# Optimization experiments

Hardware: AMD Instinct MI355X
Metric: run time of the kernel (lower is better)

## Reference

```python
import jax, jax.numpy as jnp
import numpy as np

N, DIM, K = 65536, 512, 256


def setup_inputs() -> dict:
    key = jax.random.key(0)
    k1, k2 = jax.random.split(key)
    embeddings = jax.random.normal(k1, (N, DIM), dtype=jnp.float32)
    # Centroid table produced by the (external, non-differentiable) faiss
    # k-means fit; materialized here as a learned parameter.
    centroids = jax.random.normal(k2, (K, DIM), dtype=jnp.float32)
    return {"embeddings": embeddings, "centroids": centroids, "batch_id": 0}


def reference(embeddings, centroids, batch_id):
    # Batched equivalent of the Python loop over samples:
    # for each embedding, cdist to centroids, take the 2nd-nearest centroid.
    # Squared L2 preserves the ordering of torch.cdist (monotone sqrt),
    # and the output is a gather of centroids, so math is identical.
    # d2: [N, K]
    d2 = (
        jnp.sum(embeddings * embeddings, axis=1, keepdims=True)
        - 2.0 * jnp.einsum("nd,kd->nk", embeddings, centroids)
        + jnp.sum(centroids * centroids, axis=1)
    )
    # top-2 smallest distances -> indices of nearest and 2nd-nearest centroids
    _, top2_idx = jax.lax.top_k(-d2, 2)  # [N, 2]
    hard_neg_idx = top2_idx[:, 1]  # second-nearest centroid per sample
    return centroids[hard_neg_idx]  # [N, DIM]
```

## Files before the change

### kernel.cpp

```cpp
#include <hip/hip_runtime.h>

#define N_EMB 65536
#define DIM   512
#define K_C   256
#define ROWS  128
#define NCHUNK (DIM / 32)


typedef __attribute__((ext_vector_type(4))) float        f32x4;
typedef __attribute__((ext_vector_type(8))) __bf16       bf16x8;
typedef __attribute__((ext_vector_type(8))) short        s16x8;
typedef __attribute__((ext_vector_type(4))) unsigned int u32x4;

template <class T>
__device__ inline auto mfma_bf16_t(T a, T b, f32x4 c, int)
    -> decltype(__builtin_amdgcn_mfma_f32_16x16x32_bf16(a, b, c, 0, 0, 0)) {
  return __builtin_amdgcn_mfma_f32_16x16x32_bf16(a, b, c, 0, 0, 0);
}
template <class T>
__device__ inline f32x4 mfma_bf16_t(T a, T b, f32x4 c, long) {
  return __builtin_amdgcn_mfma_f32_16x16x32_bf16(
      __builtin_bit_cast(s16x8, a), __builtin_bit_cast(s16x8, b), c, 0, 0, 0);
}
__device__ inline f32x4 MFMA(bf16x8 a, bf16x8 b, f32x4 c) {
  return mfma_bf16_t(a, b, c, 0);
}

__device__ inline unsigned umin_(unsigned a, unsigned b) { return a < b ? a : b; }
__device__ inline unsigned umax_(unsigned a, unsigned b) { return a > b ? a : b; }

__device__ inline void cvt8(const float4 a, const float4 b, u32x4& hw, u32x4& lw) {
  float v[8] = {a.x, a.y, a.z, a.w, b.x, b.y, b.z, b.w};
  unsigned h[8], l[8];
#pragma unroll
  for (int i = 0; i < 8; ++i) {
    const unsigned u  = __float_as_uint(v[i]);
    const unsigned hb = (u + 0x7FFFu + ((u >> 16) & 1u)) >> 16;
    h[i] = hb;
    const float hf = __uint_as_float(hb << 16);
    const unsigned ul = __float_as_uint(v[i] - hf);
    l[i] = (ul + 0x7FFFu + ((ul >> 16) & 1u)) >> 16;
  }
  hw = (u32x4){h[0] | (h[1] << 16), h[2] | (h[3] << 16),
               h[4] | (h[5] << 16), h[6] | (h[7] << 16)};
  lw = (u32x4){l[0] | (l[1] << 16), l[2] | (l[3] << 16),
               l[4] | (l[5] << 16), l[6] | (l[7] << 16)};
}

__device__ inline u32x4 cvt8hi(const float4 a, const float4 b) {
  float v[8] = {a.x, a.y, a.z, a.w, b.x, b.y, b.z, b.w};
  unsigned h[8];
#pragma unroll
  for (int i = 0; i < 8; ++i) {
    const unsigned u = __float_as_uint(v[i]);
    h[i] = (u + 0x7FFFu + ((u >> 16) & 1u)) >> 16;
  }
  return (u32x4){h[0] | (h[1] << 16), h[2] | (h[3] << 16),
                 h[4] | (h[5] << 16), h[6] | (h[7] << 16)};
}

__global__ void pack_centroids(const float* __restrict__ cent,
                               unsigned* __restrict__ cbh,
                               float* __restrict__ cnorm) {
  const int k    = blockIdx.x;
  const int lane = threadIdx.x;
  const float* src = cent + (size_t)k * DIM + lane * 8;
  const float4 a = *(const float4*)src;
  const float4 b = *(const float4*)(src + 4);
  const int chunk = lane >> 2, g = lane & 3;
  ((u32x4*)cbh)[((size_t)chunk * 16 + (k >> 4)) * 64 + g * 16 + (k & 15)] =
      cvt8hi(a, b);
  float s = a.x * a.x + a.y * a.y + a.z * a.z + a.w * a.w +
            b.x * b.x + b.y * b.y + b.z * b.z + b.w * b.w;
#pragma unroll
  for (int off = 32; off > 0; off >>= 1) s += __shfl_down(s, off, 64);
  if (lane == 0) cnorm[k] = s;
}

__global__ __launch_bounds__(256, 2)
void neg_sampler_main(const float* __restrict__ emb,
                      const float* __restrict__ cent,
                      const unsigned* __restrict__ cbh,
                      const float* __restrict__ cnorm,
                      float* __restrict__ out) {
  extern __shared__ char lds[];
  char* const EH = lds;
  char* const EL = lds + 8192;
  char* const CB = lds + 16384;

  const int tid  = threadIdx.x;
  const int lane = tid & 63;
  const int w    = tid >> 6;
  const int row0 = blockIdx.x * ROWS;

  f32x4 acc[2][16];
#pragma unroll
  for (int i = 0; i < 2; ++i)
#pragma unroll
    for (int j = 0; j < 16; ++j) acc[i][j] = (f32x4){0.f, 0.f, 0.f, 0.f};

  const int er = tid & 127;
  const int g0 = (tid >> 7) * 2;
  const float* const ebase = emb + (size_t)(row0 + er) * DIM;
  const int et = er >> 4, erow = er & 15;
  const int eoffA = et * 1024 + (g0 * 16 + erow) * 16;
  const int eoffB = et * 1024 + ((g0 + 1) * 16 + erow) * 16;

  float4 ev0, ev1, ev2, ev3;
  u32x4  cv0, cv1, cv2, cv3;

  auto load_chunk = [&](int c) {
    const float* p0 = ebase + c * 32 + g0 * 8;
    ev0 = *(const float4*)p0;
    ev1 = *(const float4*)(p0 + 4);
    ev2 = *(const float4*)(p0 + 8);
    ev3 = *(const float4*)(p0 + 12);
    const u32x4* cs = (const u32x4*)cbh + (size_t)c * 1024 + tid;
    cv0 = cs[0]; cv1 = cs[256]; cv2 = cs[512]; cv3 = cs[768];
  };
  auto store_chunk = [&]() {
    u32x4 hw, lw;
    cvt8(ev0, ev1, hw, lw);
    *(u32x4*)(EH + eoffA) = hw; *(u32x4*)(EL + eoffA) = lw;
    cvt8(ev2, ev3, hw, lw);
    *(u32x4*)(EH + eoffB) = hw; *(u32x4*)(EL + eoffB) = lw;
    u32x4* cd = (u32x4*)CB + tid;
    cd[0] = cv0; cd[256] = cv1; cd[512] = cv2; cd[768] = cv3;
  };

  load_chunk(0);
  for (int c = 0; c < NCHUNK; ++c) {
    if (c) __syncthreads();
    store_chunk();
    if (c < NCHUNK - 1) load_chunk(c + 1);
    asm volatile("s_waitcnt lgkmcnt(0)" ::: "memory");
    __builtin_amdgcn_sched_barrier(0);
    __builtin_amdgcn_s_barrier();
    asm volatile("" ::: "memory");

    const char* ehp = EH + (2 * w) * 1024 + lane * 16;
    const char* elp = EL + (2 * w) * 1024 + lane * 16;
    const bf16x8 eh0 = *(const bf16x8*)ehp;
    const bf16x8 eh1 = *(const bf16x8*)(ehp + 1024);
    const bf16x8 el0 = *(const bf16x8*)elp;
    const bf16x8 el1 = *(const bf16x8*)(elp + 1024);
    const char* cbp = CB + lane * 16;
#pragma unroll
    for (int ct = 0; ct < 16; ++ct) {
      const bf16x8 ch = *(const bf16x8*)(cbp + ct * 1024);
      acc[0][ct] = MFMA(eh0, ch, acc[0][ct]);
      acc[1][ct] = MFMA(eh1, ch, acc[1][ct]);
      acc[0][ct] = MFMA(el0, ch, acc[0][ct]);
      acc[1][ct] = MFMA(el1, ch, acc[1][ct]);
    }
  }
  __syncthreads();

  unsigned* top4 = (unsigned*)lds;
  const int lgrp = lane >> 4, lcol = lane & 15;
  float cnv[16];
#pragma unroll
  for (int ct = 0; ct < 16; ++ct) cnv[ct] = cnorm[ct * 16 + lcol];

#pragma unroll
  for (int rt = 0; rt < 2; ++rt) {
#pragma unroll
    for (int rg = 0; rg < 4; ++rg) {
      unsigned b0 = 0xFFFFFFFFu, b1 = b0, b2 = b0, b3 = b0;
      auto ins = [&](unsigned u) {
        b3 = umin_(b3, umax_(b2, u));
        b2 = umin_(b2, umax_(b1, u));
        b1 = umin_(b1, umax_(b0, u));
        b0 = umin_(b0, u);
      };
#pragma unroll
      for (int ct = 0; ct < 16; ++ct) {
        const float s = fmaf(-2.f, acc[rt][ct][rg], cnv[ct]);
        ins((__float_as_uint(s) & 0xFFFFFF00u) | (unsigned)(ct * 16 + lcol));
      }
#pragma unroll
      for (int off = 1; off < 16; off <<= 1) {
        const unsigned o0 = __shfl_xor(b0, off, 64);
        const unsigned o1 = __shfl_xor(b1, off, 64);
        const unsigned o2 = __shfl_xor(b2, off, 64);
        const unsigned o3 = __shfl_xor(b3, off, 64);
        ins(o0); ins(o1); ins(o2); ins(o3);
      }
      if (lcol == 0) {
        const int row = w * 32 + rt * 16 + lgrp * 4 + rg;
        *(u32x4*)(top4 + row * 4) = (u32x4){b0, b1, b2, b3};
      }
    }
  }
  __syncthreads();

  for (int rr = 0; rr < 32; ++rr) {
    const int row  = w * 32 + rr;
    const int grow = row0 + row;
    const unsigned t0 = top4[row * 4 + 0], t1 = top4[row * 4 + 1];
    const unsigned t2 = top4[row * 4 + 2], t3 = top4[row * 4 + 3];
    const int c0 = (int)(t0 & 0xFFu), c1 = (int)(t1 & 0xFFu);
    const int c2 = (int)(t2 & 0xFFu), c3 = (int)(t3 & 0xFFu);
    const int cj = lane >> 4, li = lane & 15;
    const int myc = cj == 0 ? c0 : cj == 1 ? c1 : cj == 2 ? c2 : c3;

    const float4* e4 = (const float4*)(emb + (size_t)grow * DIM);
    const float4* c4 = (const float4*)(cent + (size_t)myc * DIM);
    float d = 0.f;
#pragma unroll
    for (int i = 0; i < 8; ++i) {
      const float4 ev = e4[li + 16 * i];
      const float4 cv = c4[li + 16 * i];
      d = fmaf(ev.x, cv.x, d); d = fmaf(ev.y, cv.y, d);
      d = fmaf(ev.z, cv.z, d); d = fmaf(ev.w, cv.w, d);
    }
#pragma unroll
    for (int off = 1; off < 16; off <<= 1) d += __shfl_xor(d, off, 64);

    const float s0 = fmaf(-2.f, __shfl(d, 0, 64),  cnorm[c0]);
    const float s1 = fmaf(-2.f, __shfl(d, 16, 64), cnorm[c1]);
    const float s2 = fmaf(-2.f, __shfl(d, 32, 64), cnorm[c2]);
    const float s3 = fmaf(-2.f, __shfl(d, 48, 64), cnorm[c3]);

    float v1 = s0, v2 = 3.4e38f;
    int i1 = c0, i2 = K_C;
    auto upd = [&](float s, int c) {
      if (s < v1 || (s == v1 && c < i1)) { v2 = v1; i2 = i1; v1 = s; i1 = c; }
      else if (s < v2 || (s == v2 && c < i2)) { v2 = s; i2 = c; }
    };
    upd(s1, c1); upd(s2, c2); upd(s3, c3);

    const float4* sp = (const float4*)(cent + (size_t)i2 * DIM) + lane * 2;
    float4* op = (float4*)(out + (size_t)grow * DIM) + lane * 2;
    op[0] = sp[0];
    op[1] = sp[1];
  }
}

extern "C" void kernel_launch(void* const* d_in, const int* in_sizes, int n_in,
                              void* d_out, int out_size, void* d_ws, size_t ws_size,
                              hipStream_t stream) {
  const float* emb  = (const float*)d_in[0];
  const float* cent = (const float*)d_in[1];
  unsigned* cbh = (unsigned*)d_ws;
  float* cnorm  = (float*)((char*)d_ws + 256 * 1024);

  pack_centroids<<<K_C, 64, 0, stream>>>(cent, cbh, cnorm);
  neg_sampler_main<<<N_EMB / ROWS, 256, 32768, stream>>>(emb, cent, cbh, cnorm,
                                                         (float*)d_out);
}
```

Before: 327.8 us.

## Drop LDS staging; load embeddings and packed centroids directly into MFMA registers

The main GEMM loop no longer stages embedding hi/lo splits and centroid fragments through shared memory with block barriers. Each wave now loads its own 32 embedding rows straight into fragment-layout registers with a one-chunk prefetch, and reads the pre-packed centroid fragments directly from global/L2. The hi/lo split now truncates instead of rounding, and the refinement pass uses full-wave reductions over four candidates. This removes LDS traffic and syncs, but each wave re-reads the full centroid table from cache, and the extra registers may reduce occupancy.

```diff
diff --git a/kernel.cpp b/kernel.cpp
--- a/kernel.cpp
+++ b/kernel.cpp
@@ -3,7 +3,6 @@
 #define N_EMB 65536
 #define DIM   512
 #define K_C   256
-#define ROWS  128
 #define NCHUNK (DIM / 32)
 
 
@@ -29,22 +28,20 @@
 __device__ inline unsigned umin_(unsigned a, unsigned b) { return a < b ? a : b; }
 __device__ inline unsigned umax_(unsigned a, unsigned b) { return a > b ? a : b; }
 
-__device__ inline void cvt8(const float4 a, const float4 b, u32x4& hw, u32x4& lw) {
-  float v[8] = {a.x, a.y, a.z, a.w, b.x, b.y, b.z, b.w};
-  unsigned h[8], l[8];
-#pragma unroll
-  for (int i = 0; i < 8; ++i) {
-    const unsigned u  = __float_as_uint(v[i]);
-    const unsigned hb = (u + 0x7FFFu + ((u >> 16) & 1u)) >> 16;
-    h[i] = hb;
-    const float hf = __uint_as_float(hb << 16);
-    const unsigned ul = __float_as_uint(v[i] - hf);
-    l[i] = (ul + 0x7FFFu + ((ul >> 16) & 1u)) >> 16;
-  }
-  hw = (u32x4){h[0] | (h[1] << 16), h[2] | (h[3] << 16),
-               h[4] | (h[5] << 16), h[6] | (h[7] << 16)};
-  lw = (u32x4){l[0] | (l[1] << 16), l[2] | (l[3] << 16),
-               l[4] | (l[5] << 16), l[6] | (l[7] << 16)};
+__device__ inline void split8(const float4 a, const float4 b, u32x4& hw, u32x4& lw) {
+  const float v[8] = {a.x, a.y, a.z, a.w, b.x, b.y, b.z, b.w};
+  unsigned hp[4], lp[4];
+#pragma unroll
+  for (int i = 0; i < 4; ++i) {
+    const unsigned u0 = __float_as_uint(v[2 * i]);
+    const unsigned u1 = __float_as_uint(v[2 * i + 1]);
+    hp[i] = (u0 >> 16) | (u1 & 0xFFFF0000u);
+    const float r0 = v[2 * i]     - __uint_as_float(u0 & 0xFFFF0000u);
+    const float r1 = v[2 * i + 1] - __uint_as_float(u1 & 0xFFFF0000u);
+    lp[i] = (__float_as_uint(r0) >> 16) | (__float_as_uint(r1) & 0xFFFF0000u);
+  }
+  hw = (u32x4){hp[0], hp[1], hp[2], hp[3]};
+  lw = (u32x4){lp[0], lp[1], lp[2], lp[3]};
 }
 
 __device__ inline u32x4 cvt8hi(const float4 a, const float4 b) {
@@ -83,15 +80,13 @@
                       const unsigned* __restrict__ cbh,
                       const float* __restrict__ cnorm,
                       float* __restrict__ out) {
-  extern __shared__ char lds[];
-  char* const EH = lds;
-  char* const EL = lds + 8192;
-  char* const CB = lds + 16384;
+  __shared__ unsigned top4s[4][32][4];
 
   const int tid  = threadIdx.x;
   const int lane = tid & 63;
   const int w    = tid >> 6;
-  const int row0 = blockIdx.x * ROWS;
+  const int row0 = (blockIdx.x * 4 + w) * 32;
+  const int frow = lane & 15, fgrp = lane >> 4;
 
   f32x4 acc[2][16];
 #pragma unroll
@@ -99,65 +94,46 @@
 #pragma unroll
     for (int j = 0; j < 16; ++j) acc[i][j] = (f32x4){0.f, 0.f, 0.f, 0.f};
 
-  const int er = tid & 127;
-  const int g0 = (tid >> 7) * 2;
-  const float* const ebase = emb + (size_t)(row0 + er) * DIM;
-  const int et = er >> 4, erow = er & 15;
-  const int eoffA = et * 1024 + (g0 * 16 + erow) * 16;
-  const int eoffB = et * 1024 + ((g0 + 1) * 16 + erow) * 16;
-
-  float4 ev0, ev1, ev2, ev3;
-  u32x4  cv0, cv1, cv2, cv3;
-
-  auto load_chunk = [&](int c) {
-    const float* p0 = ebase + c * 32 + g0 * 8;
-    ev0 = *(const float4*)p0;
-    ev1 = *(const float4*)(p0 + 4);
-    ev2 = *(const float4*)(p0 + 8);
-    ev3 = *(const float4*)(p0 + 12);
-    const u32x4* cs = (const u32x4*)cbh + (size_t)c * 1024 + tid;
-    cv0 = cs[0]; cv1 = cs[256]; cv2 = cs[512]; cv3 = cs[768];
-  };
-  auto store_chunk = [&]() {
-    u32x4 hw, lw;
-    cvt8(ev0, ev1, hw, lw);
-    *(u32x4*)(EH + eoffA) = hw; *(u32x4*)(EL + eoffA) = lw;
-    cvt8(ev2, ev3, hw, lw);
-    *(u32x4*)(EH + eoffB) = hw; *(u32x4*)(EL + eoffB) = lw;
-    u32x4* cd = (u32x4*)CB + tid;
-    cd[0] = cv0; cd[256] = cv1; cd[512] = cv2; cd[768] = cv3;
-  };
-
-  load_chunk(0);
+  const float* const e0p = emb + (size_t)(row0 + frow) * DIM + fgrp * 8;
+  const float* const e1p = e0p + (size_t)16 * DIM;
+
+  float4 a0 = *(const float4*)(e0p);
+  float4 b0 = *(const float4*)(e0p + 4);
+  float4 a1 = *(const float4*)(e1p);
+  float4 b1 = *(const float4*)(e1p + 4);
+
   for (int c = 0; c < NCHUNK; ++c) {
-    if (c) __syncthreads();
-    store_chunk();
-    if (c < NCHUNK - 1) load_chunk(c + 1);
-    asm volatile("s_waitcnt lgkmcnt(0)" ::: "memory");
-    __builtin_amdgcn_sched_barrier(0);
-    __builtin_amdgcn_s_barrier();
-    asm volatile("" ::: "memory");
-
-    const char* ehp = EH + (2 * w) * 1024 + lane * 16;
-    const char* elp = EL + (2 * w) * 1024 + lane * 16;
-    const bf16x8 eh0 = *(const bf16x8*)ehp;
-    const bf16x8 eh1 = *(const bf16x8*)(ehp + 1024);
-    const bf16x8 el0 = *(const bf16x8*)elp;
-    const bf16x8 el1 = *(const bf16x8*)(elp + 1024);
-    const char* cbp = CB + lane * 16;
+    const int cn = (c + 1) & (NCHUNK - 1);
+    const float4 na0 = *(const float4*)(e0p + cn * 32);
+    const float4 nb0 = *(const float4*)(e0p + cn * 32 + 4);
+    const float4 na1 = *(const float4*)(e1p + cn * 32);
+    const float4 nb1 = *(const float4*)(e1p + cn * 32 + 4);
+
+    const u32x4* cs = (const u32x4*)cbh + (size_t)c * 1024 + lane;
+    u32x4 cc[16];
+#pragma unroll
+    for (int ct = 0; ct < 16; ++ct) cc[ct] = cs[ct * 64];
+
+    u32x4 h0, l0, h1, l1;
+    split8(a0, b0, h0, l0);
+    split8(a1, b1, h1, l1);
+    const bf16x8 eh0 = __builtin_bit_cast(bf16x8, h0);
+    const bf16x8 el0 = __builtin_bit_cast(bf16x8, l0);
+    const bf16x8 eh1 = __builtin_bit_cast(bf16x8, h1);
+    const bf16x8 el1 = __builtin_bit_cast(bf16x8, l1);
+
 #pragma unroll
     for (int ct = 0; ct < 16; ++ct) {
-      const bf16x8 ch = *(const bf16x8*)(cbp + ct * 1024);
+      const bf16x8 ch = __builtin_bit_cast(bf16x8, cc[ct]);
       acc[0][ct] = MFMA(eh0, ch, acc[0][ct]);
       acc[1][ct] = MFMA(eh1, ch, acc[1][ct]);
       acc[0][ct] = MFMA(el0, ch, acc[0][ct]);
       acc[1][ct] = MFMA(el1, ch, acc[1][ct]);
     }
-  }
-  __syncthreads();
-
-  unsigned* top4 = (unsigned*)lds;
-  const int lgrp = lane >> 4, lcol = lane & 15;
+    a0 = na0; b0 = nb0; a1 = na1; b1 = nb1;
+  }
+
+  const int lcol = lane & 15, lgrp = lane >> 4;
   float cnv[16];
 #pragma unroll
   for (int ct = 0; ct < 16; ++ct) cnv[ct] = cnorm[ct * 16 + lcol];
@@ -166,12 +142,12 @@
   for (int rt = 0; rt < 2; ++rt) {
 #pragma unroll
     for (int rg = 0; rg < 4; ++rg) {
-      unsigned b0 = 0xFFFFFFFFu, b1 = b0, b2 = b0, b3 = b0;
+      unsigned b0_ = 0xFFFFFFFFu, b1_ = b0_, b2_ = b0_, b3_ = b0_;
       auto ins = [&](unsigned u) {
-        b3 = umin_(b3, umax_(b2, u));
-        b2 = umin_(b2, umax_(b1, u));
-        b1 = umin_(b1, umax_(b0, u));
-        b0 = umin_(b0, u);
+        b3_ = umin_(b3_, umax_(b2_, u));
+        b2_ = umin_(b2_, umax_(b1_, u));
+        b1_ = umin_(b1_, umax_(b0_, u));
+        b0_ = umin_(b0_, u);
       };
 #pragma unroll
       for (int ct = 0; ct < 16; ++ct) {
@@ -180,53 +156,56 @@
       }
 #pragma unroll
       for (int off = 1; off < 16; off <<= 1) {
-        const unsigned o0 = __shfl_xor(b0, off, 64);
-        const unsigned o1 = __shfl_xor(b1, off, 64);
-        const unsigned o2 = __shfl_xor(b2, off, 64);
-        const unsigned o3 = __shfl_xor(b3, off, 64);
+        const unsigned o0 = __shfl_xor(b0_, off, 64);
+        const unsigned o1 = __shfl_xor(b1_, off, 64);
+        const unsigned o2 = __shfl_xor(b2_, off, 64);
+        const unsigned o3 = __shfl_xor(b3_, off, 64);
         ins(o0); ins(o1); ins(o2); ins(o3);
       }
       if (lcol == 0) {
-        const int row = w * 32 + rt * 16 + lgrp * 4 + rg;
-        *(u32x4*)(top4 + row * 4) = (u32x4){b0, b1, b2, b3};
+        const int rl = rt * 16 + lgrp * 4 + rg;
+        *(u32x4*)&top4s[w][rl][0] = (u32x4){b0_, b1_, b2_, b3_};
       }
     }
   }
-  __syncthreads();
 
   for (int rr = 0; rr < 32; ++rr) {
-    const int row  = w * 32 + rr;
-    const int grow = row0 + row;
-    const unsigned t0 = top4[row * 4 + 0], t1 = top4[row * 4 + 1];
-    const unsigned t2 = top4[row * 4 + 2], t3 = top4[row * 4 + 3];
-    const int c0 = (int)(t0 & 0xFFu), c1 = (int)(t1 & 0xFFu);
-    const int c2 = (int)(t2 & 0xFFu), c3 = (int)(t3 & 0xFFu);
-    const int cj = lane >> 4, li = lane & 15;
-    const int myc = cj == 0 ? c0 : cj == 1 ? c1 : cj == 2 ? c2 : c3;
-
-    const float4* e4 = (const float4*)(emb + (size_t)grow * DIM);
-    const float4* c4 = (const float4*)(cent + (size_t)myc * DIM);
-    float d = 0.f;
-#pragma unroll
-    for (int i = 0; i < 8; ++i) {
-      const float4 ev = e4[li + 16 * i];
-      const float4 cv = c4[li + 16 * i];
-      d = fmaf(ev.x, cv.x, d); d = fmaf(ev.y, cv.y, d);
-      d = fmaf(ev.z, cv.z, d); d = fmaf(ev.w, cv.w, d);
+    const int grow = row0 + rr;
+    const int c0 = (int)(top4s[w][rr][0] & 0xFFu);
+    const int c1 = (int)(top4s[w][rr][1] & 0xFFu);
+    const int c2 = (int)(top4s[w][rr][2] & 0xFFu);
+    const int c3 = (int)(top4s[w][rr][3] & 0xFFu);
+
+    const float4* e4 = (const float4*)(emb + (size_t)grow * DIM) + lane * 2;
+    const float4 ev0 = e4[0], ev1 = e4[1];
+
+    auto pdot = [&](int cj) {
+      const float4* c4 = (const float4*)(cent + (size_t)cj * DIM) + lane * 2;
+      const float4 cv0 = c4[0], cv1 = c4[1];
+      float d = ev0.x * cv0.x;
+      d = fmaf(ev0.y, cv0.y, d); d = fmaf(ev0.z, cv0.z, d); d = fmaf(ev0.w, cv0.w, d);
+      d = fmaf(ev1.x, cv1.x, d); d = fmaf(ev1.y, cv1.y, d);
+      d = fmaf(ev1.z, cv1.z, d); d = fmaf(ev1.w, cv1.w, d);
+      return d;
+    };
+    float d0 = pdot(c0), d1 = pdot(c1), d2 = pdot(c2), d3 = pdot(c3);
+#pragma unroll
+    for (int off = 1; off < 64; off <<= 1) {
+      d0 += __shfl_xor(d0, off, 64);
+      d1 += __shfl_xor(d1, off, 64);
+      d2 += __shfl_xor(d2, off, 64);
+      d3 += __shfl_xor(d3, off, 64);
     }
-#pragma unroll
-    for (int off = 1; off < 16; off <<= 1) d += __shfl_xor(d, off, 64);
-
-    const float s0 = fmaf(-2.f, __shfl(d, 0, 64),  cnorm[c0]);
-    const float s1 = fmaf(-2.f, __shfl(d, 16, 64), cnorm[c1]);
-    const float s2 = fmaf(-2.f, __shfl(d, 32, 64), cnorm[c2]);
-    const float s3 = fmaf(-2.f, __shfl(d, 48, 64), cnorm[c3]);
+    const float s0 = fmaf(-2.f, d0, cnorm[c0]);
+    const float s1 = fmaf(-2.f, d1, cnorm[c1]);
+    const float s2 = fmaf(-2.f, d2, cnorm[c2]);
+    const float s3 = fmaf(-2.f, d3, cnorm[c3]);
 
     float v1 = s0, v2 = 3.4e38f;
     int i1 = c0, i2 = K_C;
-    auto upd = [&](float s, int c) {
-      if (s < v1 || (s == v1 && c < i1)) { v2 = v1; i2 = i1; v1 = s; i1 = c; }
-      else if (s < v2 || (s == v2 && c < i2)) { v2 = s; i2 = c; }
+    auto upd = [&](float s, int ci) {
+      if (s < v1 || (s == v1 && ci < i1)) { v2 = v1; i2 = i1; v1 = s; i1 = ci; }
+      else if (s < v2 || (s == v2 && ci < i2)) { v2 = s; i2 = ci; }
     };
     upd(s1, c1); upd(s2, c2); upd(s3, c3);
 
@@ -240,12 +219,13 @@
 extern "C" void kernel_launch(void* const* d_in, const int* in_sizes, int n_in,
                               void* d_out, int out_size, void* d_ws, size_t ws_size,
                               hipStream_t stream) {
+  (void)in_sizes; (void)n_in; (void)out_size; (void)ws_size;
   const float* emb  = (const float*)d_in[0];
   const float* cent = (const float*)d_in[1];
   unsigned* cbh = (unsigned*)d_ws;
   float* cnorm  = (float*)((char*)d_ws + 256 * 1024);
 
   pack_centroids<<<K_C, 64, 0, stream>>>(cent, cbh, cnorm);
-  neg_sampler_main<<<N_EMB / ROWS, 256, 32768, stream>>>(emb, cent, cbh, cnorm,
-                                                         (float*)d_out);
-}
+  neg_sampler_main<<<N_EMB / 128, 256, 0, stream>>>(emb, cent, cbh, cnorm,
+                                                    (float*)d_out);
+}
```

New measurement: 325.5 us. No clear change (-0.7%).
